# Optimization experiments

Measured on AMD Instinct MI355X. Metric: run time of the kernel, lower is better.

## Reference

```python
import jax, jax.numpy as jnp
import numpy as np

B = 4096
N_BUS = 118
N = B * N_BUS
E_ND = 4 * N
E = E_ND + N
REF_NODE = 0
NUM_GNN_LAYERS = 10


def setup_inputs() -> dict:
    key = jax.random.key(0)
    ks = jax.random.split(key, 8)
    x = jax.random.normal(ks[0], (N, 2), dtype=jnp.float32)
    y = jax.random.normal(ks[1], (N, 1), dtype=jnp.float32)
    edge_index_no_diag = jax.random.randint(ks[2], (2, E_ND), 0, N, dtype=jnp.int64)
    edge_attr_no_diag = jax.random.normal(ks[3], (E_ND,), dtype=jnp.float32)
    edge_index = jax.random.randint(ks[4], (2, E), 0, N, dtype=jnp.int64)
    edge_attr = jax.random.normal(ks[5], (E,), dtype=jnp.float32)
    ybus = jax.random.normal(ks[6], (B, N_BUS, N_BUS), dtype=jnp.float32)
    # ensure nonzero diagonal (bus self-admittance), as in real ybus matrices
    diag = 1.0 + jax.random.uniform(ks[7], (B, N_BUS), dtype=jnp.float32)
    ii = jnp.arange(N_BUS)
    ybus = ybus.at[:, ii, ii].set(diag)
    return {"x": x, "y": y, "edge_index_no_diag": edge_index_no_diag,
            "edge_attr_no_diag": edge_attr_no_diag, "edge_index": edge_index,
            "edge_attr": edge_attr, "ybus": ybus}


def _scatter_msg(theta, edge_index, edge_w):
    # message: y_j * edge_weight * 100, aggregated (add) at target node i
    src, dst = edge_index[0], edge_index[1]
    msg = theta[src, 0] * (edge_w * 100.0)
    return jax.ops.segment_sum(msg, dst, num_segments=N)[:, None]  # [N,1]


def reference(x, y, edge_index_no_diag, edge_attr_no_diag, edge_index, edge_attr, ybus):
    p = (x[:, 0] - x[:, 1])[:, None]                               # [N,1] net power injection
    denom = (jnp.diagonal(ybus, axis1=1, axis2=2) * 100.0).reshape(-1, 1)  # [N,1]

    def gpg_layer(theta):
        aggr = _scatter_msg(theta, edge_index_no_diag, edge_attr_no_diag)
        out = (p - aggr) / denom                                   # [N,1]
        o = out.reshape(B, N_BUS)
        o = o - o[:, REF_NODE:REF_NODE + 1]                        # subtract slack-bus angle
        return o.reshape(-1, 1)

    def lc_error(theta):
        aggr = _scatter_msg(theta, edge_index, edge_attr)
        return jnp.abs(p - aggr).sum()

    theta = jnp.zeros_like(y)
    out = gpg_layer(theta)
    errors = [lc_error(out)]
    for _ in range(NUM_GNN_LAYERS):
        out = gpg_layer(out)
        errors.append(lc_error(out))
    return out, jnp.stack(errors)
```

## Files before the change

### kernel.cpp

```cpp
#include <hip/hip_runtime.h>

#define NBUS 118
#define BATCH 4096
#define NN (BATCH * NBUS)
#define END_E (4 * NN)
#define EF_E (END_E + NN)
#define NLAYERS 10

#define NBKT 236
#define SPAN_SHIFT 11
#define SPAN_MASK 2047
#define TILE 4096
#define ND_TILES (END_E / TILE)
#define F_TILES  (EF_E / TILE)
#define CAP_ND 8960
#define CAP_F  11008

#define W_ND 8
#define W_F 9
#define TAILCAP 1048576

__global__ void init_kernel(const float* __restrict__ x,
                            const float* __restrict__ ybus,
                            float* __restrict__ p,
                            float* __restrict__ denomInv,
                            int* __restrict__ cursor_nd,
                            int* __restrict__ cursor_f,
                            int* __restrict__ tailCur,
                            int4* __restrict__ ellZero,
                            float* __restrict__ errOut) {
    const int ZTOT4 = (2 * W_ND * NN + 2 * W_F * NN) / 4;
    int tid = blockIdx.x * blockDim.x + threadIdx.x;
    int stride = gridDim.x * blockDim.x;
    for (int i = tid; i < NN; i += stride) {
        float2 xi = ((const float2*)x)[i];
        p[i] = xi.x - xi.y;
        int b = i / NBUS;
        int j = i - b * NBUS;
        denomInv[i] = 1.0f / (ybus[b * (NBUS * NBUS) + j * (NBUS + 1)] * 100.0f);
    }
    for (int i = tid; i < ZTOT4; i += stride) ellZero[i] = make_int4(0, 0, 0, 0);
    if (tid < 256) {
        cursor_nd[tid] = tid * CAP_ND;
        cursor_f[tid]  = tid * CAP_F;
    }
    if (tid < 2) tailCur[tid] = 0;
    if (tid < NLAYERS + 1) errOut[tid] = 0.0f;
}

__global__ __launch_bounds__(256) void binA_kernel(
        const int* __restrict__ src_nd, const int* __restrict__ dst_nd,
        const float* __restrict__ ea_nd,
        const int* __restrict__ src_f, const int* __restrict__ dst_f,
        const float* __restrict__ ea_f,
        int* __restrict__ cursor_nd, int* __restrict__ cursor_f,
        uint2* __restrict__ stg_nd, uint2* __restrict__ stg_f) {
    __shared__ uint2 buf[TILE];
    __shared__ unsigned char sb[TILE];
    __shared__ int hist[256];
    __shared__ int scanA[256];
    __shared__ int segStart[256];
    __shared__ int segGBase[256];

    bool isF = blockIdx.x >= ND_TILES;
    int tile = isF ? (blockIdx.x - ND_TILES) : blockIdx.x;
    const int* src = isF ? src_f : src_nd;
    const int* dst = isF ? dst_f : dst_nd;
    const float* ea = isF ? ea_f : ea_nd;
    int* cursor = isF ? cursor_f : cursor_nd;
    uint2* stg = isF ? stg_f : stg_nd;
    int cap = isF ? CAP_F : CAP_ND;

    int tid = threadIdx.x;
    int base = tile * TILE;

    hist[tid] = 0;
    __syncthreads();

    #pragma unroll
    for (int k = 0; k < TILE / 256; ++k) {
        int d = dst[base + k * 256 + tid];
        atomicAdd(&hist[d >> SPAN_SHIFT], 1);
    }
    __syncthreads();

    int cnt = hist[tid];
    scanA[tid] = cnt;
    __syncthreads();
    for (int off = 1; off < 256; off <<= 1) {
        int t = (tid >= off) ? scanA[tid - off] : 0;
        __syncthreads();
        scanA[tid] += t;
        __syncthreads();
    }
    int excl = scanA[tid] - cnt;
    segStart[tid] = excl;
    hist[tid] = excl;
    if (tid < NBKT && cnt > 0) segGBase[tid] = atomicAdd(&cursor[tid], cnt);
    __syncthreads();

    #pragma unroll
    for (int k = 0; k < TILE / 256; ++k) {
        int e = base + k * 256 + tid;
        int d = dst[e];
        int bkt = d >> SPAN_SHIFT;
        int pos = atomicAdd(&hist[bkt], 1);
        unsigned dl = (unsigned)(d & SPAN_MASK);
        buf[pos] = make_uint2((unsigned)src[e] | (dl << 19),
                              (unsigned)__float_as_int(ea[e] * 100.0f));
        sb[pos] = (unsigned char)bkt;
    }
    __syncthreads();

    #pragma unroll
    for (int k = 0; k < TILE / 256; ++k) {
        int slot = k * 256 + tid;
        int bkt = sb[slot];
        int gpos = segGBase[bkt] + (slot - segStart[bkt]);
        if (gpos < (bkt + 1) * cap)
            stg[gpos] = buf[slot];
    }
}

__global__ __launch_bounds__(256) void binB_kernel(
        const uint2* __restrict__ stg_nd, const uint2* __restrict__ stg_f,
        const int* __restrict__ cursor_nd, const int* __restrict__ cursor_f,
        int2* __restrict__ ellND, int2* __restrict__ ellF,
        int2* __restrict__ tailND, int2* __restrict__ tailF,
        int* __restrict__ tailCur ) {
    __shared__ int h[2048];
    __shared__ int rk[2048];
    __shared__ int tb[2048];

    bool isF = blockIdx.x >= NBKT;
    int bb = isF ? (blockIdx.x - NBKT) : blockIdx.x;
    const uint2* stg = isF ? stg_f : stg_nd;
    int cap = isF ? CAP_F : CAP_ND;
    int W = isF ? W_F : W_ND;
    int2* ell = isF ? ellF : ellND;
    int2* tail = isF ? tailF : tailND;
    int* tc = isF ? (tailCur + 1) : tailCur;
    int cnt_all = (isF ? cursor_f[bb] : cursor_nd[bb]) - bb * cap;
    if (cnt_all > cap) cnt_all = cap;
    int stgBase = bb * cap;
    int nodeBase = bb * 2048;
    int tid = threadIdx.x;

    #pragma unroll
    for (int k = 0; k < 8; ++k) { h[k * 256 + tid] = 0; rk[k * 256 + tid] = 0; }
    __syncthreads();

    for (int i = tid; i < cnt_all; i += 256) {
        uint2 v = stg[stgBase + i];
        atomicAdd(&h[(v.x >> 19) & SPAN_MASK], 1);
    }
    __syncthreads();

    #pragma unroll
    for (int k = 0; k < 8; ++k) {
        int dl = k * 256 + tid;
        int c = h[dl];
        if (c > W) {
            int len = c - (W - 1);
            int tbase = atomicAdd(tc, len);
            if (tbase + len > TAILCAP) { tbase = 0; len = 0; }
            tb[dl] = tbase;
            ell[(W - 1) * NN + nodeBase + dl] =
                make_int2((int)(0x80000000u | (unsigned)len), tbase);
        }
    }
    __syncthreads();

    for (int i = tid; i < cnt_all; i += 256) {
        uint2 v = stg[stgBase + i];
        int dl = (v.x >> 19) & SPAN_MASK;
        int c = h[dl];
        int r = atomicAdd(&rk[dl], 1);
        int plain = (c <= W) ? c : (W - 1);
        int2 pr = make_int2((int)(v.x & 0x7FFFF), (int)v.y);
        if (r < plain) ell[r * NN + nodeBase + dl] = pr;
        else {
            int pos = tb[dl] + r - plain;
            if (pos < TAILCAP) tail[pos] = pr;
        }
    }
}

__global__ void out0_kernel(const float* __restrict__ p,
                            const float* __restrict__ denomInv,
                            float* __restrict__ out) {
    int b = blockIdx.x;
    int j = threadIdx.x;
    int i = b * NBUS + j;
    __shared__ float z0;
    float z = 0.0f;
    if (j < NBUS) z = p[i] * denomInv[i];
    if (j == 0) z0 = z;
    __syncthreads();
    if (j < NBUS) out[i] = z - z0;
}

template <bool DO_OUT>
__global__ __launch_bounds__(128) void layer_kernel(
        const int2* __restrict__ ellND, const int2* __restrict__ tailND,
        const int2* __restrict__ ellF, const int2* __restrict__ tailF,
        const float* __restrict__ cur,
        const float* __restrict__ p,
        const float* __restrict__ denomInv,
        float* __restrict__ out,
        float* __restrict__ errSlot) {
    int b = blockIdx.x;
    int j = threadIdx.x;
    int i = b * NBUS + j;
    bool act = j < NBUS;
    __shared__ float z0;
    __shared__ float ws2[2];

    float pv = 0.0f, di = 0.0f;
    float sum_nd = 0.0f, sum_f = 0.0f;
    if (act) {
        pv = p[i];
        if (DO_OUT) {
            di = denomInv[i];
            int2 e[W_ND];
            #pragma unroll
            for (int s = 0; s < W_ND - 1; ++s) e[s] = ellND[s * NN + i];
            #pragma unroll
            for (int s = 0; s < W_ND - 1; ++s)
                sum_nd += cur[e[s].x] * __int_as_float(e[s].y);
            int2 last = ellND[(W_ND - 1) * NN + i];
            if (last.x < 0) {
                int len = last.x & 0x7FFFFFFF;
                int tbase = last.y;
                for (int t = 0; t < len; ++t) {
                    int2 pr = tailND[tbase + t];
                    sum_nd += cur[pr.x] * __int_as_float(pr.y);
                }
            } else {
                sum_nd += cur[last.x] * __int_as_float(last.y);
            }
        }
        {
            int2 e[W_F];
            #pragma unroll
            for (int s = 0; s < W_F - 1; ++s) e[s] = ellF[s * NN + i];
            #pragma unroll
            for (int s = 0; s < W_F - 1; ++s)
                sum_f += cur[e[s].x] * __int_as_float(e[s].y);
            int2 last = ellF[(W_F - 1) * NN + i];
            if (last.x < 0) {
                int len = last.x & 0x7FFFFFFF;
                int tbase = last.y;
                for (int t = 0; t < len; ++t) {
                    int2 pr = tailF[tbase + t];
                    sum_f += cur[pr.x] * __int_as_float(pr.y);
                }
            } else {
                sum_f += cur[last.x] * __int_as_float(last.y);
            }
        }
    }
    if (DO_OUT) {
        float z = (pv - sum_nd) * di;
        if (j == 0) z0 = z;
        __syncthreads();
        if (act) out[i] = z - z0;
    }
    float acc = act ? fabsf(pv - sum_f) : 0.0f;
    for (int off = 32; off > 0; off >>= 1) acc += __shfl_down(acc, off, 64);
    if ((threadIdx.x & 63) == 0) ws2[threadIdx.x >> 6] = acc;
    __syncthreads();
    if (threadIdx.x == 0) atomicAdd(errSlot, ws2[0] + ws2[1]);
}

extern "C" void kernel_launch(void* const* d_in, const int* in_sizes, int n_in,
                              void* d_out, int out_size, void* d_ws, size_t ws_size,
                              hipStream_t stream) {
    const float* x     = (const float*)d_in[0];
    const int*   ei_nd = (const int*)d_in[2];
    const float* ea_nd = (const float*)d_in[3];
    const int*   ei    = (const int*)d_in[4];
    const float* ea    = (const float*)d_in[5];
    const float* ybus  = (const float*)d_in[6];

    float* out_f = (float*)d_out;
    float* errs  = out_f + NN;

    float* wsf       = (float*)d_ws;
    float* p         = wsf;          wsf += NN;
    float* denomInv  = wsf;          wsf += NN;
    float* outA      = wsf;          wsf += NN;
    float* outB      = wsf;          wsf += NN;
    int*   cursor_nd = (int*)wsf;    wsf += 256;
    int*   cursor_f  = (int*)wsf;    wsf += 256;
    int*   tailCur   = (int*)wsf;    wsf += 4;
    int2*  ellND     = (int2*)wsf;   wsf += 2LL * W_ND * NN;
    int2*  ellF      = (int2*)wsf;   wsf += 2LL * W_F * NN;
    int2*  tailND    = (int2*)wsf;   wsf += 2LL * TAILCAP;
    int2*  tailF     = (int2*)wsf;   wsf += 2LL * TAILCAP;
    uint2* stg_nd    = (uint2*)wsf;  wsf += 2LL * NBKT * CAP_ND;
    uint2* stg_f     = (uint2*)wsf;  wsf += 2LL * NBKT * CAP_F;

    const int* src_nd = ei_nd;
    const int* dst_nd = ei_nd + END_E;
    const int* src_f  = ei;
    const int* dst_f  = ei + EF_E;

    init_kernel<<<2048, 256, 0, stream>>>(x, ybus, p, denomInv,
                                          cursor_nd, cursor_f, tailCur,
                                          (int4*)ellND, errs);
    binA_kernel<<<ND_TILES + F_TILES, 256, 0, stream>>>(
        src_nd, dst_nd, ea_nd, src_f, dst_f, ea,
        cursor_nd, cursor_f, stg_nd, stg_f);
    binB_kernel<<<2 * NBKT, 256, 0, stream>>>(
        stg_nd, stg_f, cursor_nd, cursor_f,
        ellND, ellF, tailND, tailF, tailCur);

    out0_kernel<<<BATCH, 128, 0, stream>>>(p, denomInv, outA);
    const float* cur = outA;
    for (int k = 1; k <= NLAYERS; ++k) {
        float* nxt = (k == NLAYERS) ? out_f : ((k & 1) ? outB : outA);
        layer_kernel<true><<<BATCH, 128, 0, stream>>>(
            ellND, tailND, ellF, tailF, cur, p, denomInv, nxt, errs + (k - 1));
        cur = nxt;
    }
    layer_kernel<false><<<BATCH, 128, 0, stream>>>(
        ellND, tailND, ellF, tailF, cur, p, denomInv, nullptr, errs + NLAYERS);
}
```

Baseline: 1.299 ms.

## Split ELL into int index and fp16 weight arrays built via shared slabs

Replaces the int2 (src, float weight) ELL entries with separate int source and fp16 weight arrays, and packs tail length and base into one int. This cuts the bytes streamed per edge in every layer kernel. binB now assembles each 512-node slab in shared memory and writes it out with coalesced vector stores, so the global zero-fill in init goes away. The cost is weights rounded to fp16 (the edge weights are prescaled by 100), which can introduce accuracy error. It also rescans the staging buffer once per slab and caps tail length at 2047 entries.

```diff
diff --git a/kernel.cpp b/kernel.cpp
--- a/kernel.cpp
+++ b/kernel.cpp
@@ -1,4 +1,5 @@
 #include <hip/hip_runtime.h>
+#include <hip/hip_fp16.h>
 
 #define NBUS 118
 #define BATCH 4096
@@ -19,6 +20,7 @@
 #define W_ND 8
 #define W_F 9
 #define TAILCAP 1048576
+#define SLAB 512
 
 __global__ void init_kernel(const float* __restrict__ x,
                             const float* __restrict__ ybus,
@@ -27,9 +29,7 @@
                             int* __restrict__ cursor_nd,
                             int* __restrict__ cursor_f,
                             int* __restrict__ tailCur,
-                            int4* __restrict__ ellZero,
                             float* __restrict__ errOut) {
-    const int ZTOT4 = (2 * W_ND * NN + 2 * W_F * NN) / 4;
     int tid = blockIdx.x * blockDim.x + threadIdx.x;
     int stride = gridDim.x * blockDim.x;
     for (int i = tid; i < NN; i += stride) {
@@ -39,7 +39,6 @@
         int j = i - b * NBUS;
         denomInv[i] = 1.0f / (ybus[b * (NBUS * NBUS) + j * (NBUS + 1)] * 100.0f);
     }
-    for (int i = tid; i < ZTOT4; i += stride) ellZero[i] = make_int4(0, 0, 0, 0);
     if (tid < 256) {
         cursor_nd[tid] = tid * CAP_ND;
         cursor_f[tid]  = tid * CAP_F;
@@ -125,23 +124,27 @@
 __global__ __launch_bounds__(256) void binB_kernel(
         const uint2* __restrict__ stg_nd, const uint2* __restrict__ stg_f,
         const int* __restrict__ cursor_nd, const int* __restrict__ cursor_f,
-        int2* __restrict__ ellND, int2* __restrict__ ellF,
+        int* __restrict__ ellSrcND, __half* __restrict__ ellWND,
+        int* __restrict__ ellSrcF, __half* __restrict__ ellWF,
         int2* __restrict__ tailND, int2* __restrict__ tailF,
         int* __restrict__ tailCur ) {
     __shared__ int h[2048];
     __shared__ int rk[2048];
     __shared__ int tb[2048];
+    __shared__ int srcSlab[W_F * SLAB];
+    __shared__ unsigned short wSlab[W_F * SLAB];
 
     bool isF = blockIdx.x >= NBKT;
     int bb = isF ? (blockIdx.x - NBKT) : blockIdx.x;
     const uint2* stg = isF ? stg_f : stg_nd;
     int cap = isF ? CAP_F : CAP_ND;
     int W = isF ? W_F : W_ND;
-    int2* ell = isF ? ellF : ellND;
+    int* ellSrc = isF ? ellSrcF : ellSrcND;
+    __half* ellW = isF ? ellWF : ellWND;
     int2* tail = isF ? tailF : tailND;
     int* tc = isF ? (tailCur + 1) : tailCur;
-    int cnt_all = (isF ? cursor_f[bb] : cursor_nd[bb]) - bb * cap;
-    if (cnt_all > cap) cnt_all = cap;
+    int cnt = (isF ? cursor_f[bb] : cursor_nd[bb]) - bb * cap;
+    if (cnt > cap) cnt = cap;
     int stgBase = bb * cap;
     int nodeBase = bb * 2048;
     int tid = threadIdx.x;
@@ -150,7 +153,7 @@
     for (int k = 0; k < 8; ++k) { h[k * 256 + tid] = 0; rk[k * 256 + tid] = 0; }
     __syncthreads();
 
-    for (int i = tid; i < cnt_all; i += 256) {
+    for (int i = tid; i < cnt; i += 256) {
         uint2 v = stg[stgBase + i];
         atomicAdd(&h[(v.x >> 19) & SPAN_MASK], 1);
     }
@@ -163,26 +166,56 @@
         if (c > W) {
             int len = c - (W - 1);
             int tbase = atomicAdd(tc, len);
-            if (tbase + len > TAILCAP) { tbase = 0; len = 0; }
-            tb[dl] = tbase;
-            ell[(W - 1) * NN + nodeBase + dl] =
-                make_int2((int)(0x80000000u | (unsigned)len), tbase);
-        }
-    }
-    __syncthreads();
-
-    for (int i = tid; i < cnt_all; i += 256) {
-        uint2 v = stg[stgBase + i];
-        int dl = (v.x >> 19) & SPAN_MASK;
-        int c = h[dl];
-        int r = atomicAdd(&rk[dl], 1);
-        int plain = (c <= W) ? c : (W - 1);
-        int2 pr = make_int2((int)(v.x & 0x7FFFF), (int)v.y);
-        if (r < plain) ell[r * NN + nodeBase + dl] = pr;
-        else {
-            int pos = tb[dl] + r - plain;
-            if (pos < TAILCAP) tail[pos] = pr;
-        }
+            tb[dl] = (tbase + len > TAILCAP) ? -1 : tbase;
+        }
+    }
+    __syncthreads();
+
+    const int nvec = W * (SLAB / 4);
+    for (int pslab = 0; pslab < 2048 / SLAB; ++pslab) {
+        for (int idx = tid; idx < nvec; idx += 256) {
+            ((int4*)srcSlab)[idx] = make_int4(0, 0, 0, 0);
+            ((ushort4*)wSlab)[idx] = make_ushort4(0, 0, 0, 0);
+        }
+        __syncthreads();
+        for (int l = tid; l < SLAB; l += 256) {
+            int dl = pslab * SLAB + l;
+            int c = h[dl];
+            if (c > W) {
+                int tbase = tb[dl];
+                unsigned len = (tbase < 0) ? 0u : (unsigned)(c - (W - 1));
+                if (len > 2047u) len = 2047u;
+                unsigned tb_enc = (tbase < 0) ? 0u : (unsigned)tbase;
+                srcSlab[(W - 1) * SLAB + l] = (int)(0x80000000u | (len << 20) | tb_enc);
+            }
+        }
+        __syncthreads();
+        for (int i = tid; i < cnt; i += 256) {
+            uint2 v = stg[stgBase + i];
+            int dl = (v.x >> 19) & SPAN_MASK;
+            if ((dl >> 9) != pslab) continue;
+            int l = dl & (SLAB - 1);
+            int c = h[dl];
+            int r = atomicAdd(&rk[dl], 1);
+            int plain = (c <= W) ? c : (W - 1);
+            if (r < plain) {
+                srcSlab[r * SLAB + l] = (int)(v.x & 0x7FFFF);
+                wSlab[r * SLAB + l] = __half_as_ushort(__float2half(__int_as_float(v.y)));
+            } else if (tb[dl] >= 0) {
+                int pos = tb[dl] + r - plain;
+                if (pos < TAILCAP)
+                    tail[pos] = make_int2((int)(v.x & 0x7FFFF), (int)v.y);
+            }
+        }
+        __syncthreads();
+        int gbase = nodeBase + pslab * SLAB;
+        for (int idx = tid; idx < nvec; idx += 256) {
+            int row = idx >> 7;
+            int col = idx & 127;
+            ((int4*)(ellSrc + row * NN + gbase))[col] = ((int4*)srcSlab)[idx];
+            ((ushort4*)(ellW + row * NN + gbase))[col] = ((ushort4*)wSlab)[idx];
+        }
+        __syncthreads();
     }
 }
 
@@ -202,8 +235,10 @@
 
 template <bool DO_OUT>
 __global__ __launch_bounds__(128) void layer_kernel(
-        const int2* __restrict__ ellND, const int2* __restrict__ tailND,
-        const int2* __restrict__ ellF, const int2* __restrict__ tailF,
+        const int* __restrict__ ellSrcND, const __half* __restrict__ ellWND,
+        const int2* __restrict__ tailND,
+        const int* __restrict__ ellSrcF, const __half* __restrict__ ellWF,
+        const int2* __restrict__ tailF,
         const float* __restrict__ cur,
         const float* __restrict__ p,
         const float* __restrict__ denomInv,
@@ -222,41 +257,47 @@
         pv = p[i];
         if (DO_OUT) {
             di = denomInv[i];
-            int2 e[W_ND];
-            #pragma unroll
-            for (int s = 0; s < W_ND - 1; ++s) e[s] = ellND[s * NN + i];
+            int sN[W_ND - 1];
+            __half wN[W_ND - 1];
+            #pragma unroll
+            for (int s = 0; s < W_ND - 1; ++s) sN[s] = ellSrcND[s * NN + i];
+            #pragma unroll
+            for (int s = 0; s < W_ND - 1; ++s) wN[s] = ellWND[s * NN + i];
             #pragma unroll
             for (int s = 0; s < W_ND - 1; ++s)
-                sum_nd += cur[e[s].x] * __int_as_float(e[s].y);
-            int2 last = ellND[(W_ND - 1) * NN + i];
-            if (last.x < 0) {
-                int len = last.x & 0x7FFFFFFF;
-                int tbase = last.y;
+                sum_nd += cur[sN[s]] * __half2float(wN[s]);
+            int last = ellSrcND[(W_ND - 1) * NN + i];
+            if (last < 0) {
+                int len = (last >> 20) & 0x7FF;
+                int tbase = last & 0xFFFFF;
                 for (int t = 0; t < len; ++t) {
                     int2 pr = tailND[tbase + t];
                     sum_nd += cur[pr.x] * __int_as_float(pr.y);
                 }
             } else {
-                sum_nd += cur[last.x] * __int_as_float(last.y);
+                sum_nd += cur[last] * __half2float(ellWND[(W_ND - 1) * NN + i]);
             }
         }
         {
-            int2 e[W_F];
-            #pragma unroll
-            for (int s = 0; s < W_F - 1; ++s) e[s] = ellF[s * NN + i];
+            int sF[W_F - 1];
+            __half wF[W_F - 1];
+            #pragma unroll
+            for (int s = 0; s < W_F - 1; ++s) sF[s] = ellSrcF[s * NN + i];
+            #pragma unroll
+            for (int s = 0; s < W_F - 1; ++s) wF[s] = ellWF[s * NN + i];
             #pragma unroll
             for (int s = 0; s < W_F - 1; ++s)
-                sum_f += cur[e[s].x] * __int_as_float(e[s].y);
-            int2 last = ellF[(W_F - 1) * NN + i];
-            if (last.x < 0) {
-                int len = last.x & 0x7FFFFFFF;
-                int tbase = last.y;
+                sum_f += cur[sF[s]] * __half2float(wF[s]);
+            int last = ellSrcF[(W_F - 1) * NN + i];
+            if (last < 0) {
+                int len = (last >> 20) & 0x7FF;
+                int tbase = last & 0xFFFFF;
                 for (int t = 0; t < len; ++t) {
                     int2 pr = tailF[tbase + t];
                     sum_f += cur[pr.x] * __int_as_float(pr.y);
                 }
             } else {
-                sum_f += cur[last.x] * __int_as_float(last.y);
+                sum_f += cur[last] * __half2float(ellWF[(W_F - 1) * NN + i]);
             }
         }
     }
@@ -286,44 +327,47 @@
     float* out_f = (float*)d_out;
     float* errs  = out_f + NN;
 
-    float* wsf       = (float*)d_ws;
-    float* p         = wsf;          wsf += NN;
-    float* denomInv  = wsf;          wsf += NN;
-    float* outA      = wsf;          wsf += NN;
-    float* outB      = wsf;          wsf += NN;
-    int*   cursor_nd = (int*)wsf;    wsf += 256;
-    int*   cursor_f  = (int*)wsf;    wsf += 256;
-    int*   tailCur   = (int*)wsf;    wsf += 4;
-    int2*  ellND     = (int2*)wsf;   wsf += 2LL * W_ND * NN;
-    int2*  ellF      = (int2*)wsf;   wsf += 2LL * W_F * NN;
-    int2*  tailND    = (int2*)wsf;   wsf += 2LL * TAILCAP;
-    int2*  tailF     = (int2*)wsf;   wsf += 2LL * TAILCAP;
-    uint2* stg_nd    = (uint2*)wsf;  wsf += 2LL * NBKT * CAP_ND;
-    uint2* stg_f     = (uint2*)wsf;  wsf += 2LL * NBKT * CAP_F;
+    float*  wsf       = (float*)d_ws;
+    float*  p         = wsf;           wsf += NN;
+    float*  denomInv  = wsf;           wsf += NN;
+    float*  outA      = wsf;           wsf += NN;
+    float*  outB      = wsf;           wsf += NN;
+    int*    cursor_nd = (int*)wsf;     wsf += 256;
+    int*    cursor_f  = (int*)wsf;     wsf += 256;
+    int*    tailCur   = (int*)wsf;     wsf += 4;
+    int*    ellSrcND  = (int*)wsf;     wsf += (long long)W_ND * NN;
+    int*    ellSrcF   = (int*)wsf;     wsf += (long long)W_F * NN;
+    __half* ellWND    = (__half*)wsf;  wsf += (long long)W_ND * NN / 2;
+    __half* ellWF     = (__half*)wsf;  wsf += (long long)W_F * NN / 2;
+    int2*   tailND    = (int2*)wsf;    wsf += 2LL * TAILCAP;
+    int2*   tailF     = (int2*)wsf;    wsf += 2LL * TAILCAP;
+    uint2*  stg_nd    = (uint2*)wsf;   wsf += 2LL * NBKT * CAP_ND;
+    uint2*  stg_f     = (uint2*)wsf;   wsf += 2LL * NBKT * CAP_F;
 
     const int* src_nd = ei_nd;
     const int* dst_nd = ei_nd + END_E;
     const int* src_f  = ei;
     const int* dst_f  = ei + EF_E;
 
-    init_kernel<<<2048, 256, 0, stream>>>(x, ybus, p, denomInv,
-                                          cursor_nd, cursor_f, tailCur,
-                                          (int4*)ellND, errs);
+    init_kernel<<<1024, 256, 0, stream>>>(x, ybus, p, denomInv,
+                                          cursor_nd, cursor_f, tailCur, errs);
     binA_kernel<<<ND_TILES + F_TILES, 256, 0, stream>>>(
         src_nd, dst_nd, ea_nd, src_f, dst_f, ea,
         cursor_nd, cursor_f, stg_nd, stg_f);
     binB_kernel<<<2 * NBKT, 256, 0, stream>>>(
         stg_nd, stg_f, cursor_nd, cursor_f,
-        ellND, ellF, tailND, tailF, tailCur);
+        ellSrcND, ellWND, ellSrcF, ellWF, tailND, tailF, tailCur);
 
     out0_kernel<<<BATCH, 128, 0, stream>>>(p, denomInv, outA);
     const float* cur = outA;
     for (int k = 1; k <= NLAYERS; ++k) {
         float* nxt = (k == NLAYERS) ? out_f : ((k & 1) ? outB : outA);
         layer_kernel<true><<<BATCH, 128, 0, stream>>>(
-            ellND, tailND, ellF, tailF, cur, p, denomInv, nxt, errs + (k - 1));
+            ellSrcND, ellWND, tailND, ellSrcF, ellWF, tailF,
+            cur, p, denomInv, nxt, errs + (k - 1));
         cur = nxt;
     }
     layer_kernel<false><<<BATCH, 128, 0, stream>>>(
-        ellND, tailND, ellF, tailF, cur, p, denomInv, nullptr, errs + NLAYERS);
-}
+        ellSrcND, ellWND, tailND, ellSrcF, ellWF, tailF,
+        cur, p, denomInv, nullptr, errs + NLAYERS);
+}
```

Result: no change. 1.310 ms (+0.8%).
